# Kernel optimization log

Hardware: AMD Instinct MI355X
Metric: run time of the kernel (lower is better)

## Reference

```python
import jax, jax.numpy as jnp
import numpy as np

B, S, D, H, F = 4, 2048, 1024, 16, 4096
DH = D // H
EPS = 1e-6


def setup_inputs() -> dict:
    key = jax.random.key(0)
    ks = jax.random.split(key, 8)
    sc = 1.0 / np.sqrt(D)
    return {
        "x": jax.random.normal(ks[0], (B, S, D), jnp.float32),
        "wq": jax.random.normal(ks[1], (D, D), jnp.float32) * sc,
        "bq": jnp.zeros((D,), jnp.float32),
        "wk": jax.random.normal(ks[2], (D, D), jnp.float32) * sc,
        "bk": jnp.zeros((D,), jnp.float32),
        "wv": jax.random.normal(ks[3], (D, D), jnp.float32) * sc,
        "bv": jnp.zeros((D,), jnp.float32),
        "wo": jax.random.normal(ks[4], (D, D), jnp.float32) * sc,
        "bo": jnp.zeros((D,), jnp.float32),
        "w1": jax.random.normal(ks[5], (D, F), jnp.float32) * sc,
        "b1": jnp.zeros((F,), jnp.float32),
        "w2": jax.random.normal(ks[6], (F, D), jnp.float32) * (1.0 / np.sqrt(F)),
        "b2": jnp.zeros((D,), jnp.float32),
        "g1": jnp.ones((D,), jnp.float32),
        "be1": jnp.zeros((D,), jnp.float32),
        "g2": jnp.ones((D,), jnp.float32),
        "be2": jnp.zeros((D,), jnp.float32),
    }


def _layernorm(x, g, b):
    mu = jnp.mean(x, axis=-1, keepdims=True)
    var = jnp.mean(jnp.square(x - mu), axis=-1, keepdims=True)
    return (x - mu) * jax.lax.rsqrt(var + EPS) * g + b


def reference(x, wq, bq, wk, bk, wv, bv, wo, bo, w1, b1, w2, b2, g1, be1, g2, be2):
    # self-attention: q=k=v=x
    q = (x @ wq + bq).reshape(B, S, H, DH).transpose(0, 2, 1, 3)  # [B,H,S,DH]
    k = (x @ wk + bk).reshape(B, S, H, DH).transpose(0, 2, 1, 3)
    v = (x @ wv + bv).reshape(B, S, H, DH).transpose(0, 2, 1, 3)
    logits = jnp.einsum("bhqd,bhkd->bhqk", q, k) / jnp.sqrt(jnp.float32(DH))
    attn = jax.nn.softmax(logits, axis=-1)
    ctx = jnp.einsum("bhqk,bhkd->bhqd", attn, v)  # [B,H,S,DH]
    ctx = ctx.transpose(0, 2, 1, 3).reshape(B, S, D)
    attn_out = ctx @ wo + bo
    out1 = _layernorm(x + attn_out, g1, be1)
    ffn = jax.nn.relu(out1 @ w1 + b1) @ w2 + b2
    out2 = _layernorm(out1 + ffn, g2, be2)
    return out2
```

## Files before the change

kernel.cpp:

```cpp
#include <hip/hip_runtime.h>

typedef unsigned short u16;
typedef unsigned int u32;

typedef __attribute__((ext_vector_type(8))) short short8;
typedef __attribute__((ext_vector_type(4))) float floatx4;
typedef __attribute__((ext_vector_type(16))) float floatx16;
typedef __attribute__((ext_vector_type(2))) unsigned int uint2v;
typedef __attribute__((ext_vector_type(4))) unsigned int uint4v;

static __device__ __forceinline__ u16 f2b(float f) {
    union { float f; u32 i; } v; v.f = f;
    u32 r = v.i + 0x7fffu + ((v.i >> 16) & 1u);
    return (u16)(r >> 16);
}
static __device__ __forceinline__ float exp2f_hw(float x) {
    return __builtin_amdgcn_exp2f(x);
}
static __device__ __forceinline__ u32 cvtpk(float lo, float hi) {
    u32 r;
    asm("v_cvt_pk_bf16_f32 %0, %1, %2" : "=v"(r) : "v"(lo), "v"(hi));
    return r;
}

static __device__ __forceinline__ floatx4 mfma16(short8 a, short8 b, floatx4 c) {
    return __builtin_amdgcn_mfma_f32_16x16x32_bf16(a, b, c, 0, 0, 0);
}
static __device__ __forceinline__ floatx16 mfma32(short8 a, short8 b, floatx16 c) {
    return __builtin_amdgcn_mfma_f32_32x32x16_bf16(a, b, c, 0, 0, 0);
}

typedef __attribute__((address_space(1))) const void gas_void;
typedef __attribute__((address_space(3))) void las_void;
static __device__ __forceinline__ void gl_lds16(const void* g, void* l) {
    __builtin_amdgcn_global_load_lds((gas_void*)g, (las_void*)l, 16, 0, 0);
}

template<int N> static __device__ __forceinline__ void vmw() {
    if constexpr (N == 0)      asm volatile("s_waitcnt vmcnt(0)" ::: "memory");
    else if constexpr (N == 4) asm volatile("s_waitcnt vmcnt(4)" ::: "memory");
}
#define SBAR() asm volatile("s_barrier" ::: "memory")

#define B_ 4
#define S_ 2048
#define D_ 1024
#define H_ 16
#define DH_ 64
#define F_ 4096
#define QKVS 3072

#define QSCALE 0.18033688011112042f

__global__ __launch_bounds__(256) void cast_b(const float* __restrict__ in,
                                              u16* __restrict__ out, int n4) {
    int id = blockIdx.x * 256 + threadIdx.x;
    if (id < n4) {
        float4 v = ((const float4*)in)[id];
        ushort4 u;
        u.x = f2b(v.x); u.y = f2b(v.y); u.z = f2b(v.z); u.w = f2b(v.w);
        ((ushort4*)out)[id] = u;
    }
}

__global__ __launch_bounds__(256) void concat_bias(const float* __restrict__ bq,
                                                   const float* __restrict__ bk,
                                                   const float* __restrict__ bv,
                                                   float* __restrict__ o) {
    int i = blockIdx.x * 256 + threadIdx.x;
    float v;
    if (i < 1024) v = bq[i] * QSCALE;
    else if (i < 2048) v = bk[i - 1024];
    else v = bv[i - 2048];
    o[i] = v;
}

__global__ void transpose_cast(const float* __restrict__ in, u16* __restrict__ out,
                               int R, int C, float scale) {
    __shared__ float t[32][33];
    int bx = blockIdx.x;
    int by = blockIdx.y;
    int x = threadIdx.x, y = threadIdx.y;
#pragma unroll
    for (int i = 0; i < 4; ++i) {
        int r = by * 32 + y + i * 8;
        t[y + i * 8][x] = in[(size_t)r * C + bx * 32 + x];
    }
    __syncthreads();
#pragma unroll
    for (int i = 0; i < 4; ++i) {
        int c = bx * 32 + y + i * 8;
        out[(size_t)c * R + by * 32 + x] = f2b(t[x][y + i * 8] * scale);
    }
}

__global__ void transpose_v(const u16* __restrict__ qkv, u16* __restrict__ vt) {
    __shared__ u16 t[32][33];
    int bh = blockIdx.z; int b = bh >> 4, h = bh & 15;
    int s0 = blockIdx.x * 32, d0 = blockIdx.y * 32;
    int x = threadIdx.x, y = threadIdx.y;
#pragma unroll
    for (int i = 0; i < 4; ++i)
        t[y + i * 8][x] =
            qkv[(size_t)(b * S_ + s0 + y + i * 8) * QKVS + 2048 + h * DH_ + d0 + x];
    __syncthreads();
#pragma unroll
    for (int i = 0; i < 4; ++i)
        vt[((size_t)bh * DH_ + d0 + y + i * 8) * S_ + s0 + x] = t[x][y + i * 8];
}

#define MFMA16X(MH)                                                        \
    __builtin_amdgcn_s_setprio(1);                                         \
    acc[(MH)*4+0][0] = mfma16(af0, bf0, acc[(MH)*4+0][0]);                 \
    acc[(MH)*4+0][1] = mfma16(af0, bf1, acc[(MH)*4+0][1]);                 \
    acc[(MH)*4+0][2] = mfma16(af0, bf2, acc[(MH)*4+0][2]);                 \
    acc[(MH)*4+0][3] = mfma16(af0, bf3, acc[(MH)*4+0][3]);                 \
    acc[(MH)*4+1][0] = mfma16(af1, bf0, acc[(MH)*4+1][0]);                 \
    acc[(MH)*4+1][1] = mfma16(af1, bf1, acc[(MH)*4+1][1]);                 \
    acc[(MH)*4+1][2] = mfma16(af1, bf2, acc[(MH)*4+1][2]);                 \
    acc[(MH)*4+1][3] = mfma16(af1, bf3, acc[(MH)*4+1][3]);                 \
    acc[(MH)*4+2][0] = mfma16(af2, bf0, acc[(MH)*4+2][0]);                 \
    acc[(MH)*4+2][1] = mfma16(af2, bf1, acc[(MH)*4+2][1]);                 \
    acc[(MH)*4+2][2] = mfma16(af2, bf2, acc[(MH)*4+2][2]);                 \
    acc[(MH)*4+2][3] = mfma16(af2, bf3, acc[(MH)*4+2][3]);                 \
    acc[(MH)*4+3][0] = mfma16(af3, bf0, acc[(MH)*4+3][0]);                 \
    acc[(MH)*4+3][1] = mfma16(af3, bf1, acc[(MH)*4+3][1]);                 \
    acc[(MH)*4+3][2] = mfma16(af3, bf2, acc[(MH)*4+3][2]);                 \
    acc[(MH)*4+3][3] = mfma16(af3, bf3, acc[(MH)*4+3][3]);                 \
    __builtin_amdgcn_s_setprio(0);

#define PPAIR(P, KH, ST0, W0, ST1, W1) {                                   \
    int ro = l * 64 + ((((KH) * 4 + quad) ^ l7) << 3);                     \
    const u16* bBp = &smem[32768 + (P) * 16384 + wc * 4096];               \
    short8 bf0 = *(const short8*)&bBp[ro];                                 \
    short8 bf1 = *(const short8*)&bBp[ro + 1024];                          \
    short8 bf2 = *(const short8*)&bBp[ro + 2048];                          \
    short8 bf3 = *(const short8*)&bBp[ro + 3072];                          \
    {   const u16* bAp = &smem[(P) * 16384 + (wr * 2 + 0) * 4096];         \
        short8 af0 = *(const short8*)&bAp[ro];                             \
        short8 af1 = *(const short8*)&bAp[ro + 1024];                      \
        short8 af2 = *(const short8*)&bAp[ro + 2048];                      \
        short8 af3 = *(const short8*)&bAp[ro + 3072];                      \
        ST0; W0; SBAR();                                                   \
        MFMA16X(0)                                                         \
        SBAR();                                                            \
    }                                                                      \
    {   const u16* bAp = &smem[(P) * 16384 + (wr * 2 + 1) * 4096];         \
        short8 af0 = *(const short8*)&bAp[ro];                             \
        short8 af1 = *(const short8*)&bAp[ro + 1024];                      \
        short8 af2 = *(const short8*)&bAp[ro + 2048];                      \
        short8 af3 = *(const short8*)&bAp[ro + 3072];                      \
        ST1; W1; SBAR();                                                   \
        MFMA16X(1)                                                         \
        SBAR();                                                            \
    } }

__global__ __launch_bounds__(512) void gemm256(const u16* __restrict__ A,
                                               const u16* __restrict__ Bt,
                                               const float* __restrict__ bias,
                                               float* __restrict__ outF,
                                               float* __restrict__ outF2,
                                               u16* __restrict__ outB,
                                               int M, int N, int K, int klen,
                                               int relu) {
    __shared__ __align__(16) u16 smem[65536];

    int tid = threadIdx.x;
    int w = tid >> 6, lane = tid & 63, quad = lane >> 4, l = lane & 15;
    int wr = w >> 2, wc = w & 3;
    int l7 = l & 7;

    int nbN = gridDim.x, nwg = gridDim.x * gridDim.y;
    int flat = blockIdx.y * gridDim.x + blockIdx.x;
    int swz = (flat & 7) * (nwg >> 3) + (flat >> 3);
    int bM = swz / nbN, bN = swz % nbN;
    int koff = blockIdx.z * klen;

    floatx4 acc[8][4];
#pragma unroll
    for (int i = 0; i < 8; ++i)
#pragma unroll
        for (int j = 0; j < 4; ++j) acc[i][j] = (floatx4){0.f, 0.f, 0.f, 0.f};

    int rT = tid >> 3, cT = tid & 7;
    int cg8 = ((cT ^ (rT & 7)) << 3);
    const u16* gA0 = A + (size_t)(bM * 256 + rT) * K + koff + cg8;
    const u16* gB0 = Bt + (size_t)(bN * 256 + rT) * K + koff + cg8;

    auto stA = [&](int p, int ch, int t) {
        gl_lds16(gA0 + (size_t)(ch * 64) * K + t * 64,
                 (void*)&smem[p * 16384 + ch * 4096 + (w << 9)]);
    };
    auto stB = [&](int p, int hb, int t) {
        gl_lds16(gB0 + (size_t)(hb * 64) * K + t * 64,
                 (void*)&smem[32768 + p * 16384 + hb * 4096 + (w << 9)]);
    };

    stA(0, 0, 0); stA(0, 1, 0); stA(0, 2, 0); stA(0, 3, 0);
    stB(0, 0, 0); stB(0, 1, 0); stB(0, 2, 0); stB(0, 3, 0);
    stA(1, 0, 1); stA(1, 2, 1); stB(1, 0, 1); stB(1, 1, 1);
    vmw<4>(); SBAR();

    const int NI = klen >> 7;
    for (int i = 0; i < NI - 1; ++i) {
        int t1 = 2 * i + 1, t2 = 2 * i + 2, t3 = 2 * i + 3;
        PPAIR(0, 0, (stA(1,1,t1), stA(1,3,t1), stB(1,2,t1), stB(1,3,t1)),
                    ((void)0), ((void)0), ((void)0))
        PPAIR(0, 1, ((void)0), ((void)0),
                    (stA(0,0,t2), stA(0,2,t2), stB(0,0,t2), stB(0,1,t2)), vmw<4>())
        PPAIR(1, 0, (stA(0,1,t2), stA(0,3,t2), stB(0,2,t2), stB(0,3,t2)),
                    ((void)0), ((void)0), ((void)0))
        PPAIR(1, 1, ((void)0), ((void)0),
                    (stA(1,0,t3), stA(1,2,t3), stB(1,0,t3), stB(1,1,t3)), vmw<4>())
    }
    {
        int t1 = 2 * (NI - 1) + 1;
        PPAIR(0, 0, (stA(1,1,t1), stA(1,3,t1), stB(1,2,t1), stB(1,3,t1)),
                    ((void)0), ((void)0), ((void)0))
        PPAIR(0, 1, ((void)0), ((void)0), ((void)0), vmw<0>())
        PPAIR(1, 0, ((void)0), ((void)0), ((void)0), ((void)0))
        PPAIR(1, 1, ((void)0), ((void)0), ((void)0), ((void)0))
    }

    float* of = (blockIdx.z == 0) ? outF : outF2;
    const float* bp = (blockIdx.z == 0) ? bias : nullptr;
    float bv4[4];
#pragma unroll
    for (int nt = 0; nt < 4; ++nt) {
        int colg = bN * 256 + wc * 64 + nt * 16 + l;
        bv4[nt] = bp ? bp[colg] : 0.f;
    }
#pragma unroll
    for (int mt = 0; mt < 8; ++mt) {
#pragma unroll
        for (int rr = 0; rr < 4; ++rr) {
            int rowg = bM * 256 + wr * 128 + mt * 16 + quad * 4 + rr;
            size_t rb = (size_t)rowg * N + bN * 256 + wc * 64 + l;
#pragma unroll
            for (int nt = 0; nt < 4; ++nt) {
                float v = acc[mt][nt][rr] + bv4[nt];
                if (relu) v = fmaxf(v, 0.f);
                if (of) of[rb + nt * 16] = v;
                if (outB) outB[rb + nt * 16] = f2b(v);
            }
        }
    }
}

#define PACK8(sv, rb, dst) {                                                   \
    u32 pa_ = cvtpk(sv[rb + 0], sv[rb + 1]), pb_ = cvtpk(sv[rb + 4], sv[rb + 5]); \
    u32 pc_ = cvtpk(sv[rb + 2], sv[rb + 3]), pd_ = cvtpk(sv[rb + 6], sv[rb + 7]); \
    uint2v t0_ = __builtin_amdgcn_permlane32_swap(pa_, pb_, 0, 0);             \
    uint2v t1_ = __builtin_amdgcn_permlane32_swap(pc_, pd_, 0, 0);             \
    union { uint4v u; short8 s8; } cv_;                                        \
    cv_.u = (uint4v){t0_[0], t1_[0], t0_[1], t1_[1]};                          \
    dst = cv_.s8; }

__global__ __launch_bounds__(256, 2) void attn_kernel(const u16* __restrict__ qkv,
                                                      const u16* __restrict__ vt,
                                                      u16* __restrict__ ctx) {
    __shared__ __align__(16) u16 Kb[2][64 * 64];
    __shared__ __align__(16) u16 Vb[2][64 * 64];

    int bh = blockIdx.x; int b = bh >> 4, h = bh & 15;
    int tid = threadIdx.x;
    int w = tid >> 6, lane = tid & 63;
    int l32 = lane & 31, hi = lane >> 5, row7 = lane & 7;
    int qw = blockIdx.y * 256 + w * 64;

    int r = lane >> 3, c = lane & 7;
    int cs = ((c ^ r) << 3);
    const u16* gK0 = qkv + (size_t)(b * S_ + w * 16 + r) * QKVS + 1024 + h * DH_ + cs;
    const u16* gK1 = gK0 + (size_t)8 * QKVS;
    const u16* gV0 = vt + (size_t)(bh * DH_ + w * 16 + r) * S_ + cs;
    const u16* gV1 = gV0 + (size_t)8 * S_;

    auto stage = [&](int bb) {
        u16* lk = &Kb[bb][w * 16 * 64];
        u16* lv = &Vb[bb][w * 16 * 64];
        gl_lds16(gK0, lk);
        gl_lds16(gK1, lk + 8 * 64);
        gl_lds16(gV0, lv);
        gl_lds16(gV1, lv + 8 * 64);
        gK0 += (size_t)64 * QKVS; gK1 += (size_t)64 * QKVS;
        gV0 += 64; gV1 += 64;
    };

    short8 qa0, qa1, qa2, qa3, qb0, qb1, qb2, qb3;
    {
        const u16* qpA = qkv + (size_t)(b * S_ + qw + l32) * QKVS + h * DH_ + hi * 8;
        qa0 = *(const short8*)(qpA);
        qa1 = *(const short8*)(qpA + 16);
        qa2 = *(const short8*)(qpA + 32);
        qa3 = *(const short8*)(qpA + 48);
        const u16* qpB = qpA + (size_t)32 * QKVS;
        qb0 = *(const short8*)(qpB);
        qb1 = *(const short8*)(qpB + 16);
        qb2 = *(const short8*)(qpB + 32);
        qb3 = *(const short8*)(qpB + 48);
    }

    floatx16 OA0, OA1, OB0, OB1;
#pragma unroll
    for (int i = 0; i < 16; ++i) { OA0[i] = 0.f; OA1[i] = 0.f; OB0[i] = 0.f; OB1[i] = 0.f; }
    float lra0 = 0.f, lra1 = 0.f, lrb0 = 0.f, lrb1 = 0.f;

    int roff0 = l32 * 64;
    int roff1 = (32 + l32) * 64;

    stage(0);
    __syncthreads();

    const int NT = S_ / 64;
    for (int kt = 0; kt < NT; ++kt) {
        int cur = kt & 1;
        if (kt + 1 < NT) stage(cur ^ 1);

        const u16* Kc = Kb[cur];
        const u16* Vc = Vb[cur];

        short8 paA0, paA1, paA2, paA3, paB0, paB1, paB2, paB3;

        {
            floatx16 sA, sB;
#pragma unroll
            for (int i = 0; i < 16; ++i) { sA[i] = 0.f; sB[i] = 0.f; }
#pragma unroll
            for (int kc = 0; kc < 4; ++kc) {
                int ch = (((kc * 2 + hi) ^ row7) << 3);
                short8 ka = *(const short8*)&Kc[roff0 + ch];
                short8 qkA = (kc == 0) ? qa0 : (kc == 1) ? qa1 : (kc == 2) ? qa2 : qa3;
                short8 qkB = (kc == 0) ? qb0 : (kc == 1) ? qb1 : (kc == 2) ? qb2 : qb3;
                sA = mfma32(ka, qkA, sA);
                sB = mfma32(ka, qkB, sB);
            }
#pragma unroll
            for (int i = 0; i < 16; ++i) { sA[i] = exp2f_hw(sA[i]); sB[i] = exp2f_hw(sB[i]); }
#pragma unroll
            for (int i = 0; i < 16; i += 4) {
                lra0 += sA[i + 0] + sA[i + 1];
                lra1 += sA[i + 2] + sA[i + 3];
                lrb0 += sB[i + 0] + sB[i + 1];
                lrb1 += sB[i + 2] + sB[i + 3];
            }
            PACK8(sA, 0, paA0); PACK8(sA, 8, paA1);
            PACK8(sB, 0, paB0); PACK8(sB, 8, paB1);
        }

        {
            floatx16 sA, sB;
#pragma unroll
            for (int i = 0; i < 16; ++i) { sA[i] = 0.f; sB[i] = 0.f; }
#pragma unroll
            for (int kc = 0; kc < 4; ++kc) {
                int ch = (((kc * 2 + hi) ^ row7) << 3);
                short8 ka = *(const short8*)&Kc[roff1 + ch];
                short8 qkA = (kc == 0) ? qa0 : (kc == 1) ? qa1 : (kc == 2) ? qa2 : qa3;
                short8 qkB = (kc == 0) ? qb0 : (kc == 1) ? qb1 : (kc == 2) ? qb2 : qb3;
                sA = mfma32(ka, qkA, sA);
                sB = mfma32(ka, qkB, sB);
            }
#pragma unroll
            for (int i = 0; i < 16; ++i) { sA[i] = exp2f_hw(sA[i]); sB[i] = exp2f_hw(sB[i]); }
#pragma unroll
            for (int i = 0; i < 16; i += 4) {
                lra0 += sA[i + 0] + sA[i + 1];
                lra1 += sA[i + 2] + sA[i + 3];
                lrb0 += sB[i + 0] + sB[i + 1];
                lrb1 += sB[i + 2] + sB[i + 3];
            }
            PACK8(sA, 0, paA2); PACK8(sA, 8, paA3);
            PACK8(sB, 0, paB2); PACK8(sB, 8, paB3);
        }

        {
            short8 vb0 = *(const short8*)&Vc[roff0 + (((0 + hi) ^ row7) << 3)];
            OA0 = mfma32(paA0, vb0, OA0);
            OB0 = mfma32(paB0, vb0, OB0);
            short8 vb1 = *(const short8*)&Vc[roff0 + (((2 + hi) ^ row7) << 3)];
            OA0 = mfma32(paA1, vb1, OA0);
            OB0 = mfma32(paB1, vb1, OB0);
            short8 vb2 = *(const short8*)&Vc[roff0 + (((4 + hi) ^ row7) << 3)];
            OA0 = mfma32(paA2, vb2, OA0);
            OB0 = mfma32(paB2, vb2, OB0);
            short8 vb3 = *(const short8*)&Vc[roff0 + (((6 + hi) ^ row7) << 3)];
            OA0 = mfma32(paA3, vb3, OA0);
            OB0 = mfma32(paB3, vb3, OB0);
        }
        {
            short8 vb0 = *(const short8*)&Vc[roff1 + (((0 + hi) ^ row7) << 3)];
            OA1 = mfma32(paA0, vb0, OA1);
            OB1 = mfma32(paB0, vb0, OB1);
            short8 vb1 = *(const short8*)&Vc[roff1 + (((2 + hi) ^ row7) << 3)];
            OA1 = mfma32(paA1, vb1, OA1);
            OB1 = mfma32(paB1, vb1, OB1);
            short8 vb2 = *(const short8*)&Vc[roff1 + (((4 + hi) ^ row7) << 3)];
            OA1 = mfma32(paA2, vb2, OA1);
            OB1 = mfma32(paB2, vb2, OB1);
            short8 vb3 = *(const short8*)&Vc[roff1 + (((6 + hi) ^ row7) << 3)];
            OA1 = mfma32(paA3, vb3, OA1);
            OB1 = mfma32(paB3, vb3, OB1);
        }

        __syncthreads();
    }

    float lrA = lra0 + lra1;
    float lrB = lrb0 + lrb1;
    lrA += __shfl_xor(lrA, 32);
    lrB += __shfl_xor(lrB, 32);
    float invA = 1.0f / lrA;
    float invB = 1.0f / lrB;
#pragma unroll
    for (int rr = 0; rr < 16; ++rr) {
        int rowq = (rr & 3) + 8 * (rr >> 2) + 4 * hi;
        float ivA = __shfl(invA, rowq);
        float ivB = __shfl(invB, rowq);
        size_t baseA = (size_t)(b * S_ + qw + rowq) * D_ + h * DH_ + l32;
        ctx[baseA]      = f2b(OA0[rr] * ivA);
        ctx[baseA + 32] = f2b(OA1[rr] * ivA);
        size_t baseB = baseA + (size_t)32 * D_;
        ctx[baseB]      = f2b(OB0[rr] * ivB);
        ctx[baseB + 32] = f2b(OB1[rr] * ivB);
    }
}

__global__ __launch_bounds__(256) void add_ln(const float* __restrict__ a,
                                              const float* __restrict__ b,
                                              const float* __restrict__ g,
                                              const float* __restrict__ be,
                                              float* __restrict__ outF,
                                              u16* __restrict__ outB) {
    int row = blockIdx.x, tid = threadIdx.x;
    size_t base = (size_t)row * D_;
    float4 va = ((const float4*)(a + base))[tid];
    float4 vb = ((const float4*)(b + base))[tid];
    float x0 = va.x + vb.x, x1 = va.y + vb.y, x2 = va.z + vb.z, x3 = va.w + vb.w;
    float s1 = x0 + x1 + x2 + x3;
    float s2 = x0 * x0 + x1 * x1 + x2 * x2 + x3 * x3;
#pragma unroll
    for (int off = 32; off; off >>= 1) {
        s1 += __shfl_xor(s1, off);
        s2 += __shfl_xor(s2, off);
    }
    __shared__ float r1[4], r2[4];
    int w = tid >> 6, lane = tid & 63;
    if (lane == 0) { r1[w] = s1; r2[w] = s2; }
    __syncthreads();
    s1 = r1[0] + r1[1] + r1[2] + r1[3];
    s2 = r2[0] + r2[1] + r2[2] + r2[3];
    float mean = s1 * (1.0f / D_);
    float var = s2 * (1.0f / D_) - mean * mean;
    float inv = rsqrtf(var + 1e-6f);
    float4 vg = ((const float4*)g)[tid];
    float4 vbe = ((const float4*)be)[tid];
    float o0 = (x0 - mean) * inv * vg.x + vbe.x;
    float o1 = (x1 - mean) * inv * vg.y + vbe.y;
    float o2 = (x2 - mean) * inv * vg.z + vbe.z;
    float o3 = (x3 - mean) * inv * vg.w + vbe.w;
    float4 o; o.x = o0; o.y = o1; o.z = o2; o.w = o3;
    ((float4*)(outF + base))[tid] = o;
    if (outB) {
        ushort4 u;
        u.x = f2b(o0); u.y = f2b(o1); u.z = f2b(o2); u.w = f2b(o3);
        ((ushort4*)(outB + base))[tid] = u;
    }
}

__global__ __launch_bounds__(256) void add_ln3(const float* __restrict__ a,
                                               const float* __restrict__ b,
                                               const float* __restrict__ c,
                                               const float* __restrict__ g,
                                               const float* __restrict__ be,
                                               float* __restrict__ outF,
                                               u16* __restrict__ outB) {
    int row = blockIdx.x, tid = threadIdx.x;
    size_t base = (size_t)row * D_;
    float4 va = ((const float4*)(a + base))[tid];
    float4 vb = ((const float4*)(b + base))[tid];
    float4 vc = ((const float4*)(c + base))[tid];
    float x0 = va.x + vb.x + vc.x, x1 = va.y + vb.y + vc.y;
    float x2 = va.z + vb.z + vc.z, x3 = va.w + vb.w + vc.w;
    float s1 = x0 + x1 + x2 + x3;
    float s2 = x0 * x0 + x1 * x1 + x2 * x2 + x3 * x3;
#pragma unroll
    for (int off = 32; off; off >>= 1) {
        s1 += __shfl_xor(s1, off);
        s2 += __shfl_xor(s2, off);
    }
    __shared__ float r1[4], r2[4];
    int w = tid >> 6, lane = tid & 63;
    if (lane == 0) { r1[w] = s1; r2[w] = s2; }
    __syncthreads();
    s1 = r1[0] + r1[1] + r1[2] + r1[3];
    s2 = r2[0] + r2[1] + r2[2] + r2[3];
    float mean = s1 * (1.0f / D_);
    float var = s2 * (1.0f / D_) - mean * mean;
    float inv = rsqrtf(var + 1e-6f);
    float4 vg = ((const float4*)g)[tid];
    float4 vbe = ((const float4*)be)[tid];
    float o0 = (x0 - mean) * inv * vg.x + vbe.x;
    float o1 = (x1 - mean) * inv * vg.y + vbe.y;
    float o2 = (x2 - mean) * inv * vg.z + vbe.z;
    float o3 = (x3 - mean) * inv * vg.w + vbe.w;
    float4 o; o.x = o0; o.y = o1; o.z = o2; o.w = o3;
    ((float4*)(outF + base))[tid] = o;
    if (outB) {
        ushort4 u;
        u.x = f2b(o0); u.y = f2b(o1); u.z = f2b(o2); u.w = f2b(o3);
        ((ushort4*)(outB + base))[tid] = u;
    }
}

extern "C" void kernel_launch(void* const* d_in, const int* in_sizes, int n_in,
                              void* d_out, int out_size, void* d_ws, size_t ws_size,
                              hipStream_t stream) {
    const float* x   = (const float*)d_in[0];
    const float* wq  = (const float*)d_in[1];
    const float* bq  = (const float*)d_in[2];
    const float* wk  = (const float*)d_in[3];
    const float* bk  = (const float*)d_in[4];
    const float* wv  = (const float*)d_in[5];
    const float* bv  = (const float*)d_in[6];
    const float* wo  = (const float*)d_in[7];
    const float* bo  = (const float*)d_in[8];
    const float* w1  = (const float*)d_in[9];
    const float* b1  = (const float*)d_in[10];
    const float* w2  = (const float*)d_in[11];
    const float* b2  = (const float*)d_in[12];
    const float* g1  = (const float*)d_in[13];
    const float* be1 = (const float*)d_in[14];
    const float* g2  = (const float*)d_in[15];
    const float* be2 = (const float*)d_in[16];
    float* out = (float*)d_out;
    char* ws = (char*)d_ws;
    const size_t MB = 1u << 20;

    u16* xb      = (u16*)(ws + 0);
    u16* wqkvT   = (u16*)(ws + 16 * MB);
    u16* woT     = (u16*)(ws + 22 * MB);
    u16* w1T     = (u16*)(ws + 24 * MB);
    u16* w2T     = (u16*)(ws + 32 * MB);
    float* qkvb  = (float*)(ws + 40 * MB);
    u16* qkv     = (u16*)(ws + 41 * MB);
    u16* vtb     = (u16*)(ws + 89 * MB);
    u16* ctxb    = (u16*)(ws + 105 * MB);
    float* attn_out = (float*)(ws + 121 * MB);
    float* out1     = (float*)(ws + 153 * MB);
    u16* out1b   = (u16*)(ws + 0);
    float* woP1  = (float*)(ws + 41 * MB);
    u16* hidden  = (u16*)(ws + 41 * MB);
    float* ffn2p0 = (float*)(ws + 121 * MB);

    dim3 tb(32, 8);

    cast_b<<<8192, 256, 0, stream>>>(x, xb, (B_ * S_ * D_) / 4);
    transpose_cast<<<dim3(32, 32), tb, 0, stream>>>(wq, wqkvT, D_, D_, QSCALE);
    transpose_cast<<<dim3(32, 32), tb, 0, stream>>>(wk, wqkvT + 1024 * 1024, D_, D_, 1.0f);
    transpose_cast<<<dim3(32, 32), tb, 0, stream>>>(wv, wqkvT + 2048 * 1024, D_, D_, 1.0f);
    transpose_cast<<<dim3(32, 32), tb, 0, stream>>>(wo, woT, D_, D_, 1.0f);
    transpose_cast<<<dim3(128, 32), tb, 0, stream>>>(w1, w1T, D_, F_, 1.0f);
    transpose_cast<<<dim3(32, 128), tb, 0, stream>>>(w2, w2T, F_, D_, 1.0f);
    concat_bias<<<12, 256, 0, stream>>>(bq, bk, bv, qkvb);

    gemm256<<<dim3(12, 32, 1), 512, 0, stream>>>(xb, wqkvT, qkvb, nullptr, nullptr,
                                                 qkv, B_ * S_, QKVS, D_, D_, 0);
    transpose_v<<<dim3(S_ / 32, DH_ / 32, B_ * H_), tb, 0, stream>>>(qkv, vtb);

    attn_kernel<<<dim3(B_ * H_, S_ / 256), 256, 0, stream>>>(qkv, vtb, ctxb);

    gemm256<<<dim3(4, 32, 2), 512, 0, stream>>>(ctxb, woT, bo, attn_out, woP1,
                                                nullptr, B_ * S_, D_, D_, D_ / 2, 0);
    add_ln3<<<B_ * S_, 256, 0, stream>>>(x, attn_out, woP1, g1, be1, out1, out1b);

    gemm256<<<dim3(16, 32, 1), 512, 0, stream>>>(out1b, w1T, b1, nullptr, nullptr,
                                                 hidden, B_ * S_, F_, D_, D_, 1);
    gemm256<<<dim3(4, 32, 2), 512, 0, stream>>>(hidden, w2T, b2, ffn2p0, out,
                                                nullptr, B_ * S_, D_, F_, F_ / 2, 0);
    add_ln3<<<B_ * S_, 256, 0, stream>>>(out1, ffn2p0, out, g2, be2, out, nullptr);
}
```

Measured before the change: 505.9 us.

## Reschedule GEMM global-to-LDS prefetches and drop a barrier per half-step

Changes the software pipeline of the 256x256 bf16 GEMM. The B-tile loads for the next stage are moved later so they are spread across the MFMA half-steps, and the wait thresholds go from vmcnt(4) to vmcnt(2). It also removes the s_barrier that sat between issuing loads and starting the MFMAs in each half-step, aiming to cut sync stalls and smooth memory traffic. The risk is LDS hazards: B buffers are now overwritten closer to when other waves may still read them, which could race.

```diff
diff --git a/kernel.cpp b/kernel.cpp
--- a/kernel.cpp
+++ b/kernel.cpp
@@ -38,6 +38,7 @@
 
 template<int N> static __device__ __forceinline__ void vmw() {
     if constexpr (N == 0)      asm volatile("s_waitcnt vmcnt(0)" ::: "memory");
+    else if constexpr (N == 2) asm volatile("s_waitcnt vmcnt(2)" ::: "memory");
     else if constexpr (N == 4) asm volatile("s_waitcnt vmcnt(4)" ::: "memory");
 }
 #define SBAR() asm volatile("s_barrier" ::: "memory")
@@ -129,7 +130,7 @@
     acc[(MH)*4+3][3] = mfma16(af3, bf3, acc[(MH)*4+3][3]);                 \
     __builtin_amdgcn_s_setprio(0);
 
-#define PPAIR(P, KH, ST0, W0, ST1, W1) {                                   \
+#define PPAIR(P, KH, STa, Wa, STb, Wb) {                                   \
     int ro = l * 64 + ((((KH) * 4 + quad) ^ l7) << 3);                     \
     const u16* bBp = &smem[32768 + (P) * 16384 + wc * 4096];               \
     short8 bf0 = *(const short8*)&bBp[ro];                                 \
@@ -141,7 +142,7 @@
         short8 af1 = *(const short8*)&bAp[ro + 1024];                      \
         short8 af2 = *(const short8*)&bAp[ro + 2048];                      \
         short8 af3 = *(const short8*)&bAp[ro + 3072];                      \
-        ST0; W0; SBAR();                                                   \
+        STa; Wa;                                                           \
         MFMA16X(0)                                                         \
         SBAR();                                                            \
     }                                                                      \
@@ -150,7 +151,7 @@
         short8 af1 = *(const short8*)&bAp[ro + 1024];                      \
         short8 af2 = *(const short8*)&bAp[ro + 2048];                      \
         short8 af3 = *(const short8*)&bAp[ro + 3072];                      \
-        ST1; W1; SBAR();                                                   \
+        STb; Wb;                                                           \
         MFMA16X(1)                                                         \
         SBAR();                                                            \
     } }
@@ -198,25 +199,25 @@
 
     stA(0, 0, 0); stA(0, 1, 0); stA(0, 2, 0); stA(0, 3, 0);
     stB(0, 0, 0); stB(0, 1, 0); stB(0, 2, 0); stB(0, 3, 0);
-    stA(1, 0, 1); stA(1, 2, 1); stB(1, 0, 1); stB(1, 1, 1);
-    vmw<4>(); SBAR();
+    stA(1, 0, 1); stA(1, 2, 1);
+    vmw<2>(); SBAR();
 
     const int NI = klen >> 7;
-    for (int i = 0; i < NI - 1; ++i) {
-        int t1 = 2 * i + 1, t2 = 2 * i + 2, t3 = 2 * i + 3;
-        PPAIR(0, 0, (stA(1,1,t1), stA(1,3,t1), stB(1,2,t1), stB(1,3,t1)),
-                    ((void)0), ((void)0), ((void)0))
+    for (int j = 0; j < NI - 1; ++j) {
+        int to = 2 * j + 1, te = 2 * j + 2, tn = 2 * j + 3;
+        PPAIR(0, 0, (stA(1,1,to), stA(1,3,to), stB(1,0,to), stB(1,1,to)), ((void)0),
+                    (stB(1,2,to), stB(1,3,to)), ((void)0))
         PPAIR(0, 1, ((void)0), ((void)0),
-                    (stA(0,0,t2), stA(0,2,t2), stB(0,0,t2), stB(0,1,t2)), vmw<4>())
-        PPAIR(1, 0, (stA(0,1,t2), stA(0,3,t2), stB(0,2,t2), stB(0,3,t2)),
-                    ((void)0), ((void)0), ((void)0))
+                    (stA(0,0,te), stA(0,2,te)), vmw<2>())
+        PPAIR(1, 0, (stA(0,1,te), stA(0,3,te), stB(0,0,te), stB(0,1,te)), ((void)0),
+                    (stB(0,2,te), stB(0,3,te)), ((void)0))
         PPAIR(1, 1, ((void)0), ((void)0),
-                    (stA(1,0,t3), stA(1,2,t3), stB(1,0,t3), stB(1,1,t3)), vmw<4>())
+                    (stA(1,0,tn), stA(1,2,tn)), vmw<2>())
     }
     {
-        int t1 = 2 * (NI - 1) + 1;
-        PPAIR(0, 0, (stA(1,1,t1), stA(1,3,t1), stB(1,2,t1), stB(1,3,t1)),
-                    ((void)0), ((void)0), ((void)0))
+        int to = 2 * (NI - 1) + 1;
+        PPAIR(0, 0, (stA(1,1,to), stA(1,3,to), stB(1,0,to), stB(1,1,to)), ((void)0),
+                    (stB(1,2,to), stB(1,3,to)), ((void)0))
         PPAIR(0, 1, ((void)0), ((void)0), ((void)0), vmw<0>())
         PPAIR(1, 0, ((void)0), ((void)0), ((void)0), ((void)0))
         PPAIR(1, 1, ((void)0), ((void)0), ((void)0), ((void)0))
```

Result: faster. 493.1 us (-2.5%).
